# Kernel optimization log

Measured on AMD Instinct MI355X. Metric: run time of the kernel, lower is better.

Reference implementation:

```python
import jax, jax.numpy as jnp
import numpy as np

B, T_SRC, T_TGT, C_IN, C_OUT = 8, 4096, 2048, 1024, 1024
LN_EPS = 1e-5


def _prefix_mask(lens, T):
    return (jnp.arange(T)[None, :] < lens[:, None]).astype(jnp.int32)


def setup_inputs() -> dict:
    key = jax.random.key(0)
    ks = jax.random.split(key, 6)
    src = jax.random.normal(ks[0], (B, T_SRC, C_IN), dtype=jnp.float32)
    tgt = jax.random.normal(ks[1], (B, T_TGT, C_IN), dtype=jnp.float32)
    # ragged prefix lengths; first row full so src_sizes.max() == T_SRC (static result width)
    src_lens = jax.random.randint(ks[2], (B,), T_SRC // 2, T_SRC + 1).at[0].set(T_SRC)
    tgt_lens = jax.random.randint(ks[3], (B,), T_TGT // 2, T_TGT + 1).at[0].set(T_TGT)
    src_mask = _prefix_mask(src_lens, T_SRC)
    tgt_mask = _prefix_mask(tgt_lens, T_TGT)
    conv_w = jax.random.normal(ks[4], (C_OUT, C_IN), dtype=jnp.float32) * 0.02
    conv_b = jax.random.normal(ks[5], (C_OUT,), dtype=jnp.float32) * 0.02
    ln_g = jnp.ones((C_OUT,), dtype=jnp.float32)
    ln_b = jnp.zeros((C_OUT,), dtype=jnp.float32)
    return {"src": src, "src_mask": src_mask, "tgt": tgt, "tgt_mask": tgt_mask,
            "conv_w": conv_w, "conv_b": conv_b, "ln_g": ln_g, "ln_b": ln_b}


def reference(src, src_mask, tgt, tgt_mask, conv_w, conv_b, ln_g, ln_b):
    # kernel-size-1 Conv1d == per-token linear: [B,T_tgt,C_in] @ W^T + b
    y = jnp.einsum("btc,oc->bto", tgt, conv_w) + conv_b  # [B, T_tgt, C_out]

    src_sizes = src_mask.sum(-1).astype(jnp.int32)  # [B]
    tgt_sizes = tgt_mask.sum(-1).astype(jnp.int32)  # [B]

    # Batched nearest-neighbor ragged resize: out pos j maps to floor(j*tgt/src)
    j = jnp.arange(src.shape[1], dtype=jnp.int32)  # [T_src]
    safe_src = jnp.maximum(src_sizes, 1)[:, None]
    idx = (j[None, :] * tgt_sizes[:, None]) // safe_src  # [B, T_src]
    idx = jnp.clip(idx, 0, jnp.maximum(tgt_sizes, 1)[:, None] - 1)
    gathered = jnp.take_along_axis(y, idx[:, :, None], axis=1)  # [B, T_src, C_out]
    valid = (j[None, :] < src_sizes[:, None])[:, :, None]
    upsampled = jnp.where(valid, gathered, 0.0)

    # LayerNorm over channel dim (applied to all positions, incl. zero padding, as in torch)
    mu = upsampled.mean(-1, keepdims=True)
    var = jnp.mean(jnp.square(upsampled - mu), axis=-1, keepdims=True)
    out = (upsampled - mu) * jax.lax.rsqrt(var + LN_EPS) * ln_g + ln_b
    return (out, src_mask)
```

## Files before the change

kernel.cpp:

```cpp
#include <hip/hip_runtime.h>

#define NB   8
#define TSRC 4096
#define TTGT 2048
#define CH   1024

typedef __attribute__((ext_vector_type(4))) float  f32x4;
typedef __attribute__((ext_vector_type(8))) __bf16 bf16x8;
typedef __attribute__((ext_vector_type(4))) __bf16 bf16x4;

__global__ __launch_bounds__(256) void sizes_kernel(const int* __restrict__ src_mask,
                                                    const int* __restrict__ tgt_mask,
                                                    int* __restrict__ sizes) {
  const int id = blockIdx.x;
  const int b  = id & 7;
  const int* m = (id < 8) ? (src_mask + (size_t)b * TSRC) : (tgt_mask + (size_t)b * TTGT);
  const int T  = (id < 8) ? TSRC : TTGT;
  int s = 0;
  for (int i = threadIdx.x; i < T; i += 256) s += m[i];
#pragma unroll
  for (int off = 32; off > 0; off >>= 1) s += __shfl_down(s, off);
  __shared__ int red[4];
  if ((threadIdx.x & 63) == 0) red[threadIdx.x >> 6] = s;
  __syncthreads();
  if (threadIdx.x == 0) sizes[id] = red[0] + red[1] + red[2] + red[3];
}

__global__ __launch_bounds__(256, 2) void gemm_kernel(const float* __restrict__ tgt,
                                                      const float* __restrict__ W,
                                                      const float* __restrict__ bias,
                                                      const int* __restrict__ sizes,
                                                      float* __restrict__ y) {
  const int n0 = blockIdx.x * 128;
  const int m0 = blockIdx.y * 128;
  const int b  = m0 >> 11;
  const int t0 = m0 & (TTGT - 1);
  if (t0 >= sizes[8 + b]) return;

  __shared__ __bf16 As[128 * 32];
  __shared__ __bf16 Bs[128 * 32];

  const int tid  = threadIdx.x;
  const int kc   = tid & 7;
  const int r0   = tid >> 3;
  const int lane = tid & 63;
  const int wave = tid >> 6;
  const int wm   = (wave >> 1) * 64;
  const int wn   = (wave & 1) * 64;
  const int lr   = lane & 15;
  const int quad = lane >> 4;

  f32x4 acc[4][4];
  const f32x4 z = {0.f, 0.f, 0.f, 0.f};
#pragma unroll
  for (int i = 0; i < 4; ++i)
#pragma unroll
    for (int j = 0; j < 4; ++j) acc[i][j] = z;

  const float* gA = tgt + (size_t)m0 * CH;
  const float* gB = W + (size_t)n0 * CH;

  for (int kb = 0; kb < CH; kb += 32) {
#pragma unroll
    for (int rr = 0; rr < 4; ++rr) {
      const int r = r0 + rr * 32;
      const float4 va = *(const float4*)(gA + (size_t)r * CH + kb + kc * 4);
      const float4 vb = *(const float4*)(gB + (size_t)r * CH + kb + kc * 4);
      bf16x4 ua = {(__bf16)va.x, (__bf16)va.y, (__bf16)va.z, (__bf16)va.w};
      bf16x4 ub = {(__bf16)vb.x, (__bf16)vb.y, (__bf16)vb.z, (__bf16)vb.w};
      *(bf16x4*)(As + r * 32 + kc * 4) = ua;
      *(bf16x4*)(Bs + r * 32 + kc * 4) = ub;
    }
    __syncthreads();
    bf16x8 af[4], bfv[4];
#pragma unroll
    for (int i = 0; i < 4; ++i) af[i] = *(const bf16x8*)(As + (wm + i * 16 + lr) * 32 + quad * 8);
#pragma unroll
    for (int j = 0; j < 4; ++j) bfv[j] = *(const bf16x8*)(Bs + (wn + j * 16 + lr) * 32 + quad * 8);
#pragma unroll
    for (int i = 0; i < 4; ++i)
#pragma unroll
      for (int j = 0; j < 4; ++j)
        acc[i][j] = __builtin_amdgcn_mfma_f32_16x16x32_bf16(af[i], bfv[j], acc[i][j], 0, 0, 0);
    __syncthreads();
  }

#pragma unroll
  for (int i = 0; i < 4; ++i) {
    const int mrow = m0 + wm + i * 16 + quad * 4;
#pragma unroll
    for (int j = 0; j < 4; ++j) {
      const int ncol = n0 + wn + j * 16 + lr;
      const float bv = bias[ncol];
      float* yp = y + (size_t)mrow * CH + ncol;
#pragma unroll
      for (int r = 0; r < 4; ++r) yp[(size_t)r * CH] = acc[i][j][r] + bv;
    }
  }
}

__global__ __launch_bounds__(256) void ln_kernel(const float* __restrict__ y,
                                                 const int* __restrict__ sizes,
                                                 const int* __restrict__ src_mask,
                                                 const float* __restrict__ g,
                                                 const float* __restrict__ be,
                                                 float* __restrict__ out,
                                                 float* __restrict__ mask_out) {
  const int bx = blockIdx.x;
  const int b  = bx >> 12;
  const int j  = bx & (TSRC - 1);
  const int t  = threadIdx.x;
  const int ss = sizes[b];
  const int tg = sizes[8 + b];
  const bool valid = j < ss;

  float4 v = make_float4(0.f, 0.f, 0.f, 0.f);
  if (valid) {
    const int den = (ss > 0) ? ss : 1;
    int ii = (int)(((long long)j * (long long)tg) / den);
    const int hi = ((tg > 1) ? tg : 1) - 1;
    if (ii > hi) ii = hi;
    if (ii < 0) ii = 0;
    v = ((const float4*)(y + ((size_t)b * TTGT + ii) * CH))[t];
  }
  float s  = v.x + v.y + v.z + v.w;
  float sq = v.x * v.x + v.y * v.y + v.z * v.z + v.w * v.w;
#pragma unroll
  for (int off = 32; off > 0; off >>= 1) {
    s  += __shfl_down(s, off);
    sq += __shfl_down(sq, off);
  }
  __shared__ float red[8];
  __shared__ float stats[2];
  if ((t & 63) == 0) { red[t >> 6] = s; red[4 + (t >> 6)] = sq; }
  __syncthreads();
  if (t == 0) {
    const float S  = red[0] + red[1] + red[2] + red[3];
    const float Q  = red[4] + red[5] + red[6] + red[7];
    const float mu = S * (1.0f / CH);
    float var = Q * (1.0f / CH) - mu * mu;
    var = fmaxf(var, 0.0f);
    stats[0] = mu;
    stats[1] = rsqrtf(var + 1e-5f);
  }
  __syncthreads();
  const float mu = stats[0], rs = stats[1];
  const float4 gg = ((const float4*)g)[t];
  const float4 bb = ((const float4*)be)[t];
  float4 o;
  o.x = (v.x - mu) * rs * gg.x + bb.x;
  o.y = (v.y - mu) * rs * gg.y + bb.y;
  o.z = (v.z - mu) * rs * gg.z + bb.z;
  o.w = (v.w - mu) * rs * gg.w + bb.w;
  ((float4*)(out + ((size_t)b * TSRC + j) * CH))[t] = o;
  if (t == 0) mask_out[bx] = (float)src_mask[bx];
}

__global__ __launch_bounds__(256) void fallback_kernel(const float* __restrict__ tgt,
                                                       const int* __restrict__ src_mask,
                                                       const int* __restrict__ tgt_mask,
                                                       const float* __restrict__ W,
                                                       const float* __restrict__ bias,
                                                       const float* __restrict__ g,
                                                       const float* __restrict__ be,
                                                       float* __restrict__ out,
                                                       float* __restrict__ mask_out) {
  const int bx = blockIdx.x;
  const int b  = bx >> 12;
  const int j  = bx & (TSRC - 1);
  const int t  = threadIdx.x;
  int s1 = 0, s2 = 0;
  for (int i = t; i < TSRC; i += 256) s1 += src_mask[(size_t)b * TSRC + i];
  for (int i = t; i < TTGT; i += 256) s2 += tgt_mask[(size_t)b * TTGT + i];
#pragma unroll
  for (int off = 32; off > 0; off >>= 1) { s1 += __shfl_down(s1, off); s2 += __shfl_down(s2, off); }
  __shared__ int ired[8];
  if ((t & 63) == 0) { ired[t >> 6] = s1; ired[4 + (t >> 6)] = s2; }
  __syncthreads();
  const int ss = ired[0] + ired[1] + ired[2] + ired[3];
  const int tg = ired[4] + ired[5] + ired[6] + ired[7];
  const bool valid = j < ss;
  int ii = 0;
  if (valid) {
    const int den = (ss > 0) ? ss : 1;
    ii = (int)(((long long)j * (long long)tg) / den);
    const int hi = ((tg > 1) ? tg : 1) - 1;
    if (ii > hi) ii = hi;
    if (ii < 0) ii = 0;
  }
  __shared__ float trow[CH];
  const float* tr = tgt + ((size_t)b * TTGT + ii) * CH;
  for (int i = t; i < CH; i += 256) trow[i] = valid ? tr[i] : 0.0f;
  __syncthreads();
  float4 v = make_float4(0.f, 0.f, 0.f, 0.f);
  if (valid) {
    float a0 = 0.f, a1 = 0.f, a2 = 0.f, a3 = 0.f;
    const float* w0 = W + (size_t)(4 * t + 0) * CH;
    const float* w1 = W + (size_t)(4 * t + 1) * CH;
    const float* w2 = W + (size_t)(4 * t + 2) * CH;
    const float* w3 = W + (size_t)(4 * t + 3) * CH;
    for (int k = 0; k < CH; ++k) {
      const float x = trow[k];
      a0 += x * w0[k]; a1 += x * w1[k]; a2 += x * w2[k]; a3 += x * w3[k];
    }
    v.x = a0 + bias[4 * t + 0];
    v.y = a1 + bias[4 * t + 1];
    v.z = a2 + bias[4 * t + 2];
    v.w = a3 + bias[4 * t + 3];
  }
  float s  = v.x + v.y + v.z + v.w;
  float sq = v.x * v.x + v.y * v.y + v.z * v.z + v.w * v.w;
#pragma unroll
  for (int off = 32; off > 0; off >>= 1) {
    s  += __shfl_down(s, off);
    sq += __shfl_down(sq, off);
  }
  __shared__ float red[8];
  __shared__ float stats[2];
  if ((t & 63) == 0) { red[t >> 6] = s; red[4 + (t >> 6)] = sq; }
  __syncthreads();
  if (t == 0) {
    const float S  = red[0] + red[1] + red[2] + red[3];
    const float Q  = red[4] + red[5] + red[6] + red[7];
    const float mu = S * (1.0f / CH);
    float var = Q * (1.0f / CH) - mu * mu;
    var = fmaxf(var, 0.0f);
    stats[0] = mu;
    stats[1] = rsqrtf(var + 1e-5f);
  }
  __syncthreads();
  const float mu = stats[0], rs = stats[1];
  const float4 gg = ((const float4*)g)[t];
  const float4 bb = ((const float4*)be)[t];
  float4 o;
  o.x = (v.x - mu) * rs * gg.x + bb.x;
  o.y = (v.y - mu) * rs * gg.y + bb.y;
  o.z = (v.z - mu) * rs * gg.z + bb.z;
  o.w = (v.w - mu) * rs * gg.w + bb.w;
  ((float4*)(out + ((size_t)b * TSRC + j) * CH))[t] = o;
  if (t == 0) mask_out[bx] = (float)src_mask[bx];
}

extern "C" void kernel_launch(void* const* d_in, const int* in_sizes, int n_in,
                              void* d_out, int out_size, void* d_ws, size_t ws_size,
                              hipStream_t stream) {
  (void)in_sizes; (void)n_in; (void)out_size;
  const int*   src_mask = (const int*)d_in[1];
  const float* tgt      = (const float*)d_in[2];
  const int*   tgt_mask = (const int*)d_in[3];
  const float* conv_w   = (const float*)d_in[4];
  const float* conv_b   = (const float*)d_in[5];
  const float* ln_g     = (const float*)d_in[6];
  const float* ln_b     = (const float*)d_in[7];

  float* out      = (float*)d_out;
  float* mask_out = out + (size_t)NB * TSRC * CH;

  const size_t need = 256 + (size_t)NB * TTGT * CH * sizeof(float);
  if (ws_size >= need) {
    int*   sizes = (int*)d_ws;
    float* y     = (float*)((char*)d_ws + 256);
    sizes_kernel<<<16, 256, 0, stream>>>(src_mask, tgt_mask, sizes);
    gemm_kernel<<<dim3(CH / 128, (NB * TTGT) / 128), 256, 0, stream>>>(tgt, conv_w, conv_b, sizes, y);
    ln_kernel<<<NB * TSRC, 256, 0, stream>>>(y, sizes, src_mask, ln_g, ln_b, out, mask_out);
  } else {
    fallback_kernel<<<NB * TSRC, 256, 0, stream>>>(tgt, src_mask, tgt_mask, conv_w, conv_b,
                                                   ln_g, ln_b, out, mask_out);
  }
}
```

Before: 338.7 us.

## Pre-convert GEMM operands to bf16, use async LDS loads, bf16 intermediate, wave-per-row LN

Adds a conversion kernel that casts tgt rows (only valid rows) and W to bf16 and also writes the mask output. The GEMM then loads bf16 tiles straight into LDS with global_load_lds using a K tile of 64, and stores y as bf16. LayerNorm now handles one row per wave with vectorized bf16 loads and single-pass mean and variance. The aim is to cut GEMM global traffic and conversion work in the inner loop and to halve intermediate traffic. In exchange it adds an extra pass over tgt and loses precision in y; the old fp32 path stays as a fallback when the workspace is too small.

```diff
diff --git a/kernel.cpp b/kernel.cpp
--- a/kernel.cpp
+++ b/kernel.cpp
@@ -4,10 +4,16 @@
 #define TSRC 4096
 #define TTGT 2048
 #define CH   1024
+#define BK   64
 
 typedef __attribute__((ext_vector_type(4))) float  f32x4;
 typedef __attribute__((ext_vector_type(8))) __bf16 bf16x8;
 typedef __attribute__((ext_vector_type(4))) __bf16 bf16x4;
+
+__device__ __forceinline__ void async16(const void* g, void* l) {
+  __builtin_amdgcn_global_load_lds((const __attribute__((address_space(1))) void*)g,
+                                   (__attribute__((address_space(3))) void*)l, 16, 0, 0);
+}
 
 __global__ __launch_bounds__(256) void sizes_kernel(const int* __restrict__ src_mask,
                                                     const int* __restrict__ tgt_mask,
@@ -26,20 +32,185 @@
   if (threadIdx.x == 0) sizes[id] = red[0] + red[1] + red[2] + red[3];
 }
 
-__global__ __launch_bounds__(256, 2) void gemm_kernel(const float* __restrict__ tgt,
+__global__ __launch_bounds__(256) void convert_kernel(const float* __restrict__ tgt,
                                                       const float* __restrict__ W,
-                                                      const float* __restrict__ bias,
                                                       const int* __restrict__ sizes,
-                                                      float* __restrict__ y) {
+                                                      const int* __restrict__ src_mask,
+                                                      __bf16* __restrict__ Abf,
+                                                      __bf16* __restrict__ Wbf,
+                                                      float* __restrict__ mask_out) {
+  const int bx = blockIdx.x;
+  const int t  = threadIdx.x;
+  if (bx < (NB * TSRC) / 256) {
+    const int i = bx * 256 + t;
+    mask_out[i] = (float)src_mask[i];
+  }
+  if (bx < NB * TTGT) {
+    const int b = bx >> 11;
+    const int r = bx & (TTGT - 1);
+    if (r >= sizes[8 + b]) return;
+    const float4 v = ((const float4*)(tgt + (size_t)bx * CH))[t];
+    bf16x4 u = {(__bf16)v.x, (__bf16)v.y, (__bf16)v.z, (__bf16)v.w};
+    *(bf16x4*)(Abf + (size_t)bx * CH + t * 4) = u;
+  } else {
+    const int r = bx - NB * TTGT;
+    const float4 v = ((const float4*)(W + (size_t)r * CH))[t];
+    bf16x4 u = {(__bf16)v.x, (__bf16)v.y, (__bf16)v.z, (__bf16)v.w};
+    *(bf16x4*)(Wbf + (size_t)r * CH + t * 4) = u;
+  }
+}
+
+__global__ __launch_bounds__(256) void gemm_kernel(const __bf16* __restrict__ A,
+                                                   const __bf16* __restrict__ Bw,
+                                                   const float* __restrict__ bias,
+                                                   const int* __restrict__ sizes,
+                                                   __bf16* __restrict__ y) {
   const int n0 = blockIdx.x * 128;
   const int m0 = blockIdx.y * 128;
   const int b  = m0 >> 11;
   const int t0 = m0 & (TTGT - 1);
   if (t0 >= sizes[8 + b]) return;
 
+  __shared__ __bf16 As[128 * BK];
+  __shared__ __bf16 Bs[128 * BK];
+
+  const int tid  = threadIdx.x;
+  const int lane = tid & 63;
+  const int wave = tid >> 6;
+  const int wm   = (wave >> 1) * 64;
+  const int wn   = (wave & 1) * 64;
+  const int lr   = lane & 15;
+  const int quad = lane >> 4;
+
+  const int srow = tid >> 3;
+  const int scol = (tid & 7) * 8;
+  const __bf16* gA = A  + ((size_t)(m0 + srow)) * CH + scol;
+  const __bf16* gB = Bw + ((size_t)(n0 + srow)) * CH + scol;
+  __bf16* lA = As + tid * 8;
+  __bf16* lB = Bs + tid * 8;
+
+  f32x4 acc[4][4];
+  const f32x4 z = {0.f, 0.f, 0.f, 0.f};
+#pragma unroll
+  for (int i = 0; i < 4; ++i)
+#pragma unroll
+    for (int j = 0; j < 4; ++j) acc[i][j] = z;
+
+  for (int kb = 0; kb < CH; kb += BK) {
+#pragma unroll
+    for (int q = 0; q < 4; ++q) {
+      async16(gA + (size_t)q * 32 * CH + kb, lA + q * 2048);
+      async16(gB + (size_t)q * 32 * CH + kb, lB + q * 2048);
+    }
+    __syncthreads();
+#pragma unroll
+    for (int ko = 0; ko < 2; ++ko) {
+      bf16x8 af[4], bf[4];
+#pragma unroll
+      for (int i = 0; i < 4; ++i)
+        af[i] = *(const bf16x8*)(As + (wm + i * 16 + lr) * BK + ko * 32 + quad * 8);
+#pragma unroll
+      for (int j = 0; j < 4; ++j)
+        bf[j] = *(const bf16x8*)(Bs + (wn + j * 16 + lr) * BK + ko * 32 + quad * 8);
+#pragma unroll
+      for (int i = 0; i < 4; ++i)
+#pragma unroll
+        for (int j = 0; j < 4; ++j)
+          acc[i][j] = __builtin_amdgcn_mfma_f32_16x16x32_bf16(af[i], bf[j], acc[i][j], 0, 0, 0);
+    }
+    __syncthreads();
+  }
+
+#pragma unroll
+  for (int i = 0; i < 4; ++i) {
+    const int mrow = m0 + wm + i * 16 + quad * 4;
+#pragma unroll
+    for (int j = 0; j < 4; ++j) {
+      const int ncol = n0 + wn + j * 16 + lr;
+      const float bv = bias[ncol];
+      __bf16* yp = y + (size_t)mrow * CH + ncol;
+#pragma unroll
+      for (int r = 0; r < 4; ++r) yp[(size_t)r * CH] = (__bf16)(acc[i][j][r] + bv);
+    }
+  }
+}
+
+__global__ __launch_bounds__(256) void ln_kernel(const __bf16* __restrict__ y,
+                                                 const int* __restrict__ sizes,
+                                                 const float* __restrict__ g,
+                                                 const float* __restrict__ be,
+                                                 float* __restrict__ out) {
+  const int wid = (blockIdx.x * 256 + threadIdx.x) >> 6;
+  const int l   = threadIdx.x & 63;
+#pragma unroll
+  for (int rr = 0; rr < 4; ++rr) {
+    const int row = wid + rr * 8192;
+    const int b   = row >> 12;
+    const int j   = row & (TSRC - 1);
+    const int ss  = sizes[b];
+    const int tg  = sizes[8 + b];
+    float v[16];
+    if (j < ss) {
+      const int den = (ss > 0) ? ss : 1;
+      int ii = (int)(((long long)j * (long long)tg) / den);
+      const int hi = ((tg > 1) ? tg : 1) - 1;
+      ii = (ii > hi) ? hi : ((ii < 0) ? 0 : ii);
+      const __bf16* yr = y + ((size_t)b * TTGT + ii) * CH;
+      const bf16x8 u0 = *(const bf16x8*)(yr + l * 8);
+      const bf16x8 u1 = *(const bf16x8*)(yr + 512 + l * 8);
+#pragma unroll
+      for (int k = 0; k < 8; ++k) { v[k] = (float)u0[k]; v[8 + k] = (float)u1[k]; }
+    } else {
+#pragma unroll
+      for (int k = 0; k < 16; ++k) v[k] = 0.f;
+    }
+    float s = 0.f, q = 0.f;
+#pragma unroll
+    for (int k = 0; k < 16; ++k) { s += v[k]; q += v[k] * v[k]; }
+#pragma unroll
+    for (int off = 32; off > 0; off >>= 1) {
+      s += __shfl_xor(s, off);
+      q += __shfl_xor(q, off);
+    }
+    const float mu = s * (1.0f / CH);
+    float var = q * (1.0f / CH) - mu * mu;
+    var = fmaxf(var, 0.0f);
+    const float rs = rsqrtf(var + 1e-5f);
+    float* orow = out + (size_t)row * CH;
+#pragma unroll
+    for (int h = 0; h < 2; ++h) {
+      const int base = h * 512 + l * 8;
+      const float4 g0 = *(const float4*)(g + base);
+      const float4 g1 = *(const float4*)(g + base + 4);
+      const float4 b0 = *(const float4*)(be + base);
+      const float4 b1 = *(const float4*)(be + base + 4);
+      float4 o0, o1;
+      o0.x = (v[h * 8 + 0] - mu) * rs * g0.x + b0.x;
+      o0.y = (v[h * 8 + 1] - mu) * rs * g0.y + b0.y;
+      o0.z = (v[h * 8 + 2] - mu) * rs * g0.z + b0.z;
+      o0.w = (v[h * 8 + 3] - mu) * rs * g0.w + b0.w;
+      o1.x = (v[h * 8 + 4] - mu) * rs * g1.x + b1.x;
+      o1.y = (v[h * 8 + 5] - mu) * rs * g1.y + b1.y;
+      o1.z = (v[h * 8 + 6] - mu) * rs * g1.z + b1.z;
+      o1.w = (v[h * 8 + 7] - mu) * rs * g1.w + b1.w;
+      *(float4*)(orow + base)     = o0;
+      *(float4*)(orow + base + 4) = o1;
+    }
+  }
+}
+
+__global__ __launch_bounds__(256, 2) void gemm_f32_kernel(const float* __restrict__ tgt,
+                                                          const float* __restrict__ W,
+                                                          const float* __restrict__ bias,
+                                                          const int* __restrict__ sizes,
+                                                          float* __restrict__ y) {
+  const int n0 = blockIdx.x * 128;
+  const int m0 = blockIdx.y * 128;
+  const int b  = m0 >> 11;
+  const int t0 = m0 & (TTGT - 1);
+  if (t0 >= sizes[8 + b]) return;
   __shared__ __bf16 As[128 * 32];
   __shared__ __bf16 Bs[128 * 32];
-
   const int tid  = threadIdx.x;
   const int kc   = tid & 7;
   const int r0   = tid >> 3;
@@ -49,17 +220,14 @@
   const int wn   = (wave & 1) * 64;
   const int lr   = lane & 15;
   const int quad = lane >> 4;
-
   f32x4 acc[4][4];
   const f32x4 z = {0.f, 0.f, 0.f, 0.f};
 #pragma unroll
   for (int i = 0; i < 4; ++i)
 #pragma unroll
     for (int j = 0; j < 4; ++j) acc[i][j] = z;
-
   const float* gA = tgt + (size_t)m0 * CH;
   const float* gB = W + (size_t)n0 * CH;
-
   for (int kb = 0; kb < CH; kb += 32) {
 #pragma unroll
     for (int rr = 0; rr < 4; ++rr) {
@@ -84,7 +252,6 @@
         acc[i][j] = __builtin_amdgcn_mfma_f32_16x16x32_bf16(af[i], bfv[j], acc[i][j], 0, 0, 0);
     __syncthreads();
   }
-
 #pragma unroll
   for (int i = 0; i < 4; ++i) {
     const int mrow = m0 + wm + i * 16 + quad * 4;
@@ -99,13 +266,13 @@
   }
 }
 
-__global__ __launch_bounds__(256) void ln_kernel(const float* __restrict__ y,
-                                                 const int* __restrict__ sizes,
-                                                 const int* __restrict__ src_mask,
-                                                 const float* __restrict__ g,
-                                                 const float* __restrict__ be,
-                                                 float* __restrict__ out,
-                                                 float* __restrict__ mask_out) {
+__global__ __launch_bounds__(256) void ln_f32_kernel(const float* __restrict__ y,
+                                                     const int* __restrict__ sizes,
+                                                     const int* __restrict__ src_mask,
+                                                     const float* __restrict__ g,
+                                                     const float* __restrict__ be,
+                                                     float* __restrict__ out,
+                                                     float* __restrict__ mask_out) {
   const int bx = blockIdx.x;
   const int b  = bx >> 12;
   const int j  = bx & (TSRC - 1);
@@ -113,7 +280,6 @@
   const int ss = sizes[b];
   const int tg = sizes[8 + b];
   const bool valid = j < ss;
-
   float4 v = make_float4(0.f, 0.f, 0.f, 0.f);
   if (valid) {
     const int den = (ss > 0) ? ss : 1;
@@ -256,13 +422,30 @@
   float* out      = (float*)d_out;
   float* mask_out = out + (size_t)NB * TSRC * CH;
 
-  const size_t need = 256 + (size_t)NB * TTGT * CH * sizeof(float);
-  if (ws_size >= need) {
+  const size_t M       = (size_t)NB * TTGT;
+  const size_t off_abf = 256;
+  const size_t off_wbf = off_abf + M * CH * 2;
+  const size_t off_y   = off_wbf + (size_t)CH * CH * 2;
+  const size_t need2   = off_y + M * CH * 2;
+  const size_t need1   = 256 + M * CH * 4;
+
+  if (ws_size >= need2) {
+    int*    sizes = (int*)d_ws;
+    __bf16* Abf   = (__bf16*)((char*)d_ws + off_abf);
+    __bf16* Wbf   = (__bf16*)((char*)d_ws + off_wbf);
+    __bf16* y     = (__bf16*)((char*)d_ws + off_y);
+    sizes_kernel<<<16, 256, 0, stream>>>(src_mask, tgt_mask, sizes);
+    convert_kernel<<<NB * TTGT + CH, 256, 0, stream>>>(tgt, conv_w, sizes, src_mask,
+                                                       Abf, Wbf, mask_out);
+    gemm_kernel<<<dim3(CH / 128, (NB * TTGT) / 128), 256, 0, stream>>>(Abf, Wbf, conv_b,
+                                                                       sizes, y);
+    ln_kernel<<<2048, 256, 0, stream>>>(y, sizes, ln_g, ln_b, out);
+  } else if (ws_size >= need1) {
     int*   sizes = (int*)d_ws;
     float* y     = (float*)((char*)d_ws + 256);
     sizes_kernel<<<16, 256, 0, stream>>>(src_mask, tgt_mask, sizes);
-    gemm_kernel<<<dim3(CH / 128, (NB * TTGT) / 128), 256, 0, stream>>>(tgt, conv_w, conv_b, sizes, y);
-    ln_kernel<<<NB * TSRC, 256, 0, stream>>>(y, sizes, src_mask, ln_g, ln_b, out, mask_out);
+    gemm_f32_kernel<<<dim3(CH / 128, (NB * TTGT) / 128), 256, 0, stream>>>(tgt, conv_w, conv_b, sizes, y);
+    ln_f32_kernel<<<NB * TSRC, 256, 0, stream>>>(y, sizes, src_mask, ln_g, ln_b, out, mask_out);
   } else {
     fallback_kernel<<<NB * TSRC, 256, 0, stream>>>(tgt, src_mask, tgt_mask, conv_w, conv_b,
                                                    ln_g, ln_b, out, mask_out);
```

After: 320.5 us. 1.06x faster.
